# Optimization experiments

Measured on AMD Instinct MI355X. Metric: run time of the kernel, lower is better.

Reference implementation:

```python
import jax, jax.numpy as jnp
import numpy as np

N = 100000   # active voxels
C = 64       # inplanes
K3 = 27      # kernel^dim = 3^3 rulebook offsets
EPS = 1e-4   # scn.BatchNormReLU default eps


def setup_inputs() -> dict:
    key = jax.random.key(0)
    ks = jax.random.split(key, 14)
    features = jax.random.normal(ks[0], (N, C), dtype=jnp.float32)
    raw = jax.random.randint(ks[1], (N, K3), 0, 2 * N)
    neighbor_idx = jnp.where(raw < N, raw, -1).astype(jnp.int32)
    # center offset of a submanifold conv is always the site itself
    neighbor_idx = neighbor_idx.at[:, K3 // 2].set(jnp.arange(N, dtype=jnp.int32))

    def bn_params(k1, k2, k3, k4):
        gamma = 1.0 + 0.1 * jax.random.normal(k1, (C,), dtype=jnp.float32)
        beta = 0.1 * jax.random.normal(k2, (C,), dtype=jnp.float32)
        mean = 0.05 * jax.random.normal(k3, (C,), dtype=jnp.float32)
        var = 1.0 + 0.1 * jax.random.uniform(k4, (C,), dtype=jnp.float32)
        return gamma, beta, mean, var

    g1, b1, m1, v1 = bn_params(ks[2], ks[3], ks[4], ks[5])
    g2, b2, m2, v2 = bn_params(ks[6], ks[7], ks[8], ks[9])
    scale = 1.0 / np.sqrt(K3 * C)
    W1 = scale * jax.random.normal(ks[10], (K3, C, C), dtype=jnp.float32)
    W2 = scale * jax.random.normal(ks[11], (K3, C, C), dtype=jnp.float32)
    return {
        "features": features, "neighbor_idx": neighbor_idx,
        "gamma1": g1, "beta1": b1, "mean1": m1, "var1": v1, "W1": W1,
        "gamma2": g2, "beta2": b2, "mean2": m2, "var2": v2, "W2": W2,
    }


def _bn_relu(x, gamma, beta, mean, var):
    # eval-mode BatchNorm fused with ReLU, per channel
    return jax.nn.relu((x - mean) * jax.lax.rsqrt(var + EPS) * gamma + beta)


def _subm_conv(x, neighbor_idx, W):
    # gather neighbor features per rulebook offset, masked sum of per-offset GEMMs
    valid = neighbor_idx >= 0                       # [N, K3]
    g = x[jnp.where(valid, neighbor_idx, 0)]        # [N, K3, C]
    g = jnp.where(valid[..., None], g, 0.0)
    return jnp.einsum('nkc,kcd->nd', g, W)          # [N, C]


def reference(features, neighbor_idx, gamma1, beta1, mean1, var1, W1,
              gamma2, beta2, mean2, var2, W2):
    y = _bn_relu(features, gamma1, beta1, mean1, var1)
    y = _subm_conv(y, neighbor_idx, W1)
    y = _bn_relu(y, gamma2, beta2, mean2, var2)
    y = _subm_conv(y, neighbor_idx, W2)
    return features + y
```

## Files before the change

### kernel.cpp

```cpp
#include <hip/hip_runtime.h>
#include <hip/hip_bf16.h>

#define NS 100000
#define CC 64
#define K3 27
#define EPSV 1e-4f

typedef __attribute__((ext_vector_type(4))) float f32x4;
typedef __attribute__((ext_vector_type(8))) short bf16x8;

__device__ __forceinline__ short f2bf(float f) {
    union { float f; unsigned u; } uf; uf.f = f;
    unsigned r = (uf.u + 0x7fffu + ((uf.u >> 16) & 1u)) >> 16;
    return (short)r;
}

__global__ void prep_coeffs(const float* __restrict__ g1, const float* __restrict__ b1,
                            const float* __restrict__ m1, const float* __restrict__ v1,
                            const float* __restrict__ g2, const float* __restrict__ b2,
                            const float* __restrict__ m2, const float* __restrict__ v2,
                            float* __restrict__ coeffs) {
    int t = threadIdx.x;
    int ch = t & 63;
    if (t < 64) {
        float s = g1[ch] * rsqrtf(v1[ch] + EPSV);
        coeffs[ch] = s;
        coeffs[64 + ch] = b1[ch] - m1[ch] * s;
    } else {
        float s = g2[ch] * rsqrtf(v2[ch] + EPSV);
        coeffs[128 + ch] = s;
        coeffs[192 + ch] = b2[ch] - m2[ch] * s;
    }
}

__global__ void pack_w(const float* __restrict__ W1, const float* __restrict__ W2,
                       short* __restrict__ Wp1, short* __restrict__ Wp2) {
    int t = blockIdx.x * blockDim.x + threadIdx.x;
    if (t >= 2 * K3 * 8 * 64) return;
    int lane = t & 63;
    int f = t >> 6;
    int which = f / (K3 * 8);
    int f2 = f % (K3 * 8);
    int k = f2 >> 3, kc = (f2 >> 2) & 1, t4 = f2 & 3;
    const float* W = which ? W2 : W1;
    short* Wp = which ? Wp2 : Wp1;
    int col = t4 * 16 + (lane & 15);
    int kr0 = kc * 32 + 8 * (lane >> 4);
    bf16x8 v;
#pragma unroll
    for (int j = 0; j < 8; ++j) v[j] = f2bf(W[(k * CC + kr0 + j) * CC + col]);
    *(bf16x8*)(Wp + ((long)f2 * 64 + lane) * 8) = v;
}

__global__ void bn1_to_bf16(const float* __restrict__ x, const float* __restrict__ coeffs,
                            short* __restrict__ X1, short* __restrict__ X2) {
    int tid = blockIdx.x * blockDim.x + threadIdx.x;
    if (tid < NS * 8) {
        int ch8 = (tid & 7) * 8;
        const float* px = x + (long)tid * 8;
        float4 u = *(const float4*)px;
        float4 w = *(const float4*)(px + 4);
        float o[8] = {u.x, u.y, u.z, u.w, w.x, w.y, w.z, w.w};
        bf16x8 r;
#pragma unroll
        for (int j = 0; j < 8; ++j) {
            float s = coeffs[ch8 + j], bi = coeffs[64 + ch8 + j];
            float y = fmaxf(fmaf(o[j], s, bi), 0.f);
            r[j] = f2bf(y);
        }
        *(bf16x8*)(X1 + (long)tid * 8) = r;
    }
    if (blockIdx.x == 0 && threadIdx.x < 64) {
        X1[(long)NS * 64 + threadIdx.x] = 0;
        X2[(long)NS * 64 + threadIdx.x] = 0;
    }
}

template <int PHASE>
__global__ __launch_bounds__(256) void subm_conv(
    const short* __restrict__ Xg,
    const int* __restrict__ nb,
    const short* __restrict__ Wp,
    const float* __restrict__ coeffs,
    const float* __restrict__ feat,
    short* __restrict__ Xout,
    float* __restrict__ yout)
{
    int lane = threadIdx.x & 63;
    int wv = blockIdx.x * 4 + (threadIdx.x >> 6);
    int base = wv * 32;
    if (base >= NS) return;
    int r15 = lane & 15, hi = lane >> 4;
    int site0 = base + r15;
    int site1 = base + 16 + r15;

    f32x4 acc[2][4] = {};
    const bf16x8* wpv = (const bf16x8*)Wp;

    for (int k = 0; k < K3; ++k) {
        int i0 = nb[site0 * K3 + k];
        int i1 = nb[site1 * K3 + k];
        int q0 = (i0 < 0) ? NS : i0;
        int q1 = (i1 < 0) ? NS : i1;
        const short* p0 = Xg + (long)q0 * 64 + hi * 8;
        const short* p1 = Xg + (long)q1 * 64 + hi * 8;
        bf16x8 a00 = *(const bf16x8*)p0;
        bf16x8 a01 = *(const bf16x8*)(p0 + 32);
        bf16x8 a10 = *(const bf16x8*)p1;
        bf16x8 a11 = *(const bf16x8*)(p1 + 32);
        const bf16x8* bp = wpv + (long)k * 8 * 64 + lane;
#pragma unroll
        for (int t4 = 0; t4 < 4; ++t4) {
            bf16x8 b0 = bp[t4 * 64];
            bf16x8 b1 = bp[(4 + t4) * 64];
            acc[0][t4] = __builtin_amdgcn_mfma_f32_16x16x32_bf16(a00, b0, acc[0][t4], 0, 0, 0);
            acc[1][t4] = __builtin_amdgcn_mfma_f32_16x16x32_bf16(a10, b0, acc[1][t4], 0, 0, 0);
            acc[0][t4] = __builtin_amdgcn_mfma_f32_16x16x32_bf16(a01, b1, acc[0][t4], 0, 0, 0);
            acc[1][t4] = __builtin_amdgcn_mfma_f32_16x16x32_bf16(a11, b1, acc[1][t4], 0, 0, 0);
        }
    }

#pragma unroll
    for (int mt = 0; mt < 2; ++mt) {
#pragma unroll
        for (int t4 = 0; t4 < 4; ++t4) {
            int col = t4 * 16 + r15;
            float sc = 0.f, bi = 0.f;
            if (PHASE == 1) { sc = coeffs[128 + col]; bi = coeffs[192 + col]; }
#pragma unroll
            for (int r = 0; r < 4; ++r) {
                int row = base + mt * 16 + hi * 4 + r;
                long off = (long)row * 64 + col;
                float v = acc[mt][t4][r];
                if (PHASE == 1) {
                    float y = fmaxf(fmaf(v, sc, bi), 0.f);
                    Xout[off] = f2bf(y);
                } else {
                    yout[off] = feat[off] + v;
                }
            }
        }
    }
}

extern "C" void kernel_launch(void* const* d_in, const int* in_sizes, int n_in,
                              void* d_out, int out_size, void* d_ws, size_t ws_size,
                              hipStream_t stream) {
    const float* feat = (const float*)d_in[0];
    const int*   nb   = (const int*)d_in[1];
    const float* g1 = (const float*)d_in[2];
    const float* b1 = (const float*)d_in[3];
    const float* m1 = (const float*)d_in[4];
    const float* v1 = (const float*)d_in[5];
    const float* W1 = (const float*)d_in[6];
    const float* g2 = (const float*)d_in[7];
    const float* b2 = (const float*)d_in[8];
    const float* m2 = (const float*)d_in[9];
    const float* v2 = (const float*)d_in[10];
    const float* W2 = (const float*)d_in[11];
    float* out = (float*)d_out;

    char* ws = (char*)d_ws;
    short* X1 = (short*)ws;
    short* X2 = (short*)(ws + 12802048);
    short* Wp1 = (short*)(ws + 25604096);
    short* Wp2 = (short*)(ws + 25604096 + 221184);
    float* coeffs = (float*)(ws + 25604096 + 2 * 221184);

    prep_coeffs<<<1, 128, 0, stream>>>(g1, b1, m1, v1, g2, b2, m2, v2, coeffs);
    pack_w<<<108, 256, 0, stream>>>(W1, W2, Wp1, Wp2);
    bn1_to_bf16<<<3125, 256, 0, stream>>>(feat, coeffs, X1, X2);
    subm_conv<1><<<782, 256, 0, stream>>>(X1, nb, Wp1, coeffs, nullptr, X2, nullptr);
    subm_conv<2><<<782, 256, 0, stream>>>(X2, nb, Wp2, coeffs, feat, nullptr, out);
}
```

Measured before the change: 270.5 us.

## Split rulebook offsets across waves with LDS reduction and merge prep kernels

Each block now handles 32 sites, and its four waves each take a strided subset of the 27 offsets. Partial accumulators are reduced through shared memory before a vectorized epilogue. Neighbor indices are prefetched up front, and the prep, weight-pack and BN1 kernels are merged into one launch, with BN coefficients computed inline. This raises parallelism and grid size (3125 blocks instead of 782) to better hide gather latency. The cost is 32KB of LDS per block, a __syncthreads, and one padded wasted iteration for the waves whose offset index reaches 27 or more.

```diff
diff --git a/kernel.cpp b/kernel.cpp
--- a/kernel.cpp
+++ b/kernel.cpp
@@ -5,6 +5,8 @@
 #define CC 64
 #define K3 27
 #define EPSV 1e-4f
+#define NBLK 3125
+#define PACKB 108
 
 typedef __attribute__((ext_vector_type(4))) float f32x4;
 typedef __attribute__((ext_vector_type(8))) short bf16x8;
@@ -15,100 +17,108 @@
     return (short)r;
 }
 
-__global__ void prep_coeffs(const float* __restrict__ g1, const float* __restrict__ b1,
-                            const float* __restrict__ m1, const float* __restrict__ v1,
-                            const float* __restrict__ g2, const float* __restrict__ b2,
-                            const float* __restrict__ m2, const float* __restrict__ v2,
-                            float* __restrict__ coeffs) {
-    int t = threadIdx.x;
-    int ch = t & 63;
-    if (t < 64) {
-        float s = g1[ch] * rsqrtf(v1[ch] + EPSV);
-        coeffs[ch] = s;
-        coeffs[64 + ch] = b1[ch] - m1[ch] * s;
-    } else {
-        float s = g2[ch] * rsqrtf(v2[ch] + EPSV);
-        coeffs[128 + ch] = s;
-        coeffs[192 + ch] = b2[ch] - m2[ch] * s;
-    }
-}
-
-__global__ void pack_w(const float* __restrict__ W1, const float* __restrict__ W2,
-                       short* __restrict__ Wp1, short* __restrict__ Wp2) {
-    int t = blockIdx.x * blockDim.x + threadIdx.x;
-    if (t >= 2 * K3 * 8 * 64) return;
-    int lane = t & 63;
-    int f = t >> 6;
-    int which = f / (K3 * 8);
-    int f2 = f % (K3 * 8);
-    int k = f2 >> 3, kc = (f2 >> 2) & 1, t4 = f2 & 3;
-    const float* W = which ? W2 : W1;
-    short* Wp = which ? Wp2 : Wp1;
-    int col = t4 * 16 + (lane & 15);
-    int kr0 = kc * 32 + 8 * (lane >> 4);
-    bf16x8 v;
-#pragma unroll
-    for (int j = 0; j < 8; ++j) v[j] = f2bf(W[(k * CC + kr0 + j) * CC + col]);
-    *(bf16x8*)(Wp + ((long)f2 * 64 + lane) * 8) = v;
-}
-
-__global__ void bn1_to_bf16(const float* __restrict__ x, const float* __restrict__ coeffs,
-                            short* __restrict__ X1, short* __restrict__ X2) {
-    int tid = blockIdx.x * blockDim.x + threadIdx.x;
-    if (tid < NS * 8) {
+__global__ __launch_bounds__(256) void prepare(
+    const float* __restrict__ x,
+    const float* __restrict__ g1, const float* __restrict__ b1,
+    const float* __restrict__ m1, const float* __restrict__ v1,
+    const float* __restrict__ W1, const float* __restrict__ W2,
+    short* __restrict__ X1, short* __restrict__ X2,
+    short* __restrict__ Wp1, short* __restrict__ Wp2)
+{
+    int blk = blockIdx.x;
+    if (blk < NBLK) {
+        int tid = blk * 256 + threadIdx.x;
         int ch8 = (tid & 7) * 8;
+        float4 ga = *(const float4*)(g1 + ch8), gb = *(const float4*)(g1 + ch8 + 4);
+        float4 ba = *(const float4*)(b1 + ch8), bb = *(const float4*)(b1 + ch8 + 4);
+        float4 ma = *(const float4*)(m1 + ch8), mb = *(const float4*)(m1 + ch8 + 4);
+        float4 va = *(const float4*)(v1 + ch8), vb = *(const float4*)(v1 + ch8 + 4);
+        float g[8] = {ga.x,ga.y,ga.z,ga.w,gb.x,gb.y,gb.z,gb.w};
+        float b[8] = {ba.x,ba.y,ba.z,ba.w,bb.x,bb.y,bb.z,bb.w};
+        float m[8] = {ma.x,ma.y,ma.z,ma.w,mb.x,mb.y,mb.z,mb.w};
+        float vv[8] = {va.x,va.y,va.z,va.w,vb.x,vb.y,vb.z,vb.w};
         const float* px = x + (long)tid * 8;
         float4 u = *(const float4*)px;
         float4 w = *(const float4*)(px + 4);
-        float o[8] = {u.x, u.y, u.z, u.w, w.x, w.y, w.z, w.w};
+        float o[8] = {u.x,u.y,u.z,u.w,w.x,w.y,w.z,w.w};
         bf16x8 r;
 #pragma unroll
         for (int j = 0; j < 8; ++j) {
-            float s = coeffs[ch8 + j], bi = coeffs[64 + ch8 + j];
-            float y = fmaxf(fmaf(o[j], s, bi), 0.f);
-            r[j] = f2bf(y);
+            float s = g[j] * rsqrtf(vv[j] + EPSV);
+            float bi = b[j] - m[j] * s;
+            r[j] = f2bf(fmaxf(fmaf(o[j], s, bi), 0.f));
         }
         *(bf16x8*)(X1 + (long)tid * 8) = r;
-    }
-    if (blockIdx.x == 0 && threadIdx.x < 64) {
-        X1[(long)NS * 64 + threadIdx.x] = 0;
-        X2[(long)NS * 64 + threadIdx.x] = 0;
+        if (blk == 0 && threadIdx.x < 64) {
+            X1[(long)NS * 64 + threadIdx.x] = 0;
+            X2[(long)NS * 64 + threadIdx.x] = 0;
+        }
+    } else {
+        int t = (blk - NBLK) * 256 + threadIdx.x;
+        if (t >= 2 * K3 * 8 * 64) return;
+        int lane = t & 63;
+        int f = t >> 6;
+        int which = f / (K3 * 8);
+        int f2 = f % (K3 * 8);
+        int k = f2 >> 3, kc = (f2 >> 2) & 1, t4 = f2 & 3;
+        const float* W = which ? W2 : W1;
+        short* Wp = which ? Wp2 : Wp1;
+        int col = t4 * 16 + (lane & 15);
+        int kr0 = kc * 32 + 8 * (lane >> 4);
+        bf16x8 v;
+#pragma unroll
+        for (int j = 0; j < 8; ++j) v[j] = f2bf(W[(k * CC + kr0 + j) * CC + col]);
+        *(bf16x8*)(Wp + ((long)f2 * 64 + lane) * 8) = v;
     }
 }
 
 template <int PHASE>
-__global__ __launch_bounds__(256) void subm_conv(
+__global__ __launch_bounds__(256, 4) void subm_conv(
     const short* __restrict__ Xg,
     const int* __restrict__ nb,
     const short* __restrict__ Wp,
-    const float* __restrict__ coeffs,
+    const float* __restrict__ g2, const float* __restrict__ b2,
+    const float* __restrict__ m2, const float* __restrict__ v2,
     const float* __restrict__ feat,
-    short* __restrict__ Xout,
-    float* __restrict__ yout)
+    short* __restrict__ Xout, float* __restrict__ yout)
 {
+    __shared__ float red[4][32][64];
+    __shared__ float s2c[64], b2c[64];
     int lane = threadIdx.x & 63;
-    int wv = blockIdx.x * 4 + (threadIdx.x >> 6);
-    int base = wv * 32;
-    if (base >= NS) return;
+    int w = threadIdx.x >> 6;
+    int base = blockIdx.x * 32;
     int r15 = lane & 15, hi = lane >> 4;
-    int site0 = base + r15;
-    int site1 = base + 16 + r15;
+    int site0 = base + r15, site1 = base + 16 + r15;
+
+    if (PHASE == 1 && threadIdx.x < 64) {
+        float s = g2[threadIdx.x] * rsqrtf(v2[threadIdx.x] + EPSV);
+        s2c[threadIdx.x] = s;
+        b2c[threadIdx.x] = b2[threadIdx.x] - m2[threadIdx.x] * s;
+    }
+
+    int q0[7], q1[7];
+#pragma unroll
+    for (int j = 0; j < 7; ++j) {
+        int k = w + 4 * j;
+        int i0 = (k < K3) ? nb[site0 * K3 + k] : -1;
+        int i1 = (k < K3) ? nb[site1 * K3 + k] : -1;
+        q0[j] = (i0 < 0) ? NS : i0;
+        q1[j] = (i1 < 0) ? NS : i1;
+    }
 
     f32x4 acc[2][4] = {};
     const bf16x8* wpv = (const bf16x8*)Wp;
-
-    for (int k = 0; k < K3; ++k) {
-        int i0 = nb[site0 * K3 + k];
-        int i1 = nb[site1 * K3 + k];
-        int q0 = (i0 < 0) ? NS : i0;
-        int q1 = (i1 < 0) ? NS : i1;
-        const short* p0 = Xg + (long)q0 * 64 + hi * 8;
-        const short* p1 = Xg + (long)q1 * 64 + hi * 8;
+#pragma unroll
+    for (int j = 0; j < 7; ++j) {
+        int k = w + 4 * j;
+        int kk = (k < K3) ? k : 0;
+        const short* p0 = Xg + (long)q0[j] * 64 + hi * 8;
+        const short* p1 = Xg + (long)q1[j] * 64 + hi * 8;
         bf16x8 a00 = *(const bf16x8*)p0;
         bf16x8 a01 = *(const bf16x8*)(p0 + 32);
         bf16x8 a10 = *(const bf16x8*)p1;
         bf16x8 a11 = *(const bf16x8*)(p1 + 32);
-        const bf16x8* bp = wpv + (long)k * 8 * 64 + lane;
+        const bf16x8* bp = wpv + (long)kk * 8 * 64 + lane;
 #pragma unroll
         for (int t4 = 0; t4 < 4; ++t4) {
             bf16x8 b0 = bp[t4 * 64];
@@ -121,25 +131,36 @@
     }
 
 #pragma unroll
-    for (int mt = 0; mt < 2; ++mt) {
+    for (int mt = 0; mt < 2; ++mt)
 #pragma unroll
-        for (int t4 = 0; t4 < 4; ++t4) {
-            int col = t4 * 16 + r15;
-            float sc = 0.f, bi = 0.f;
-            if (PHASE == 1) { sc = coeffs[128 + col]; bi = coeffs[192 + col]; }
+        for (int t4 = 0; t4 < 4; ++t4)
 #pragma unroll
-            for (int r = 0; r < 4; ++r) {
-                int row = base + mt * 16 + hi * 4 + r;
-                long off = (long)row * 64 + col;
-                float v = acc[mt][t4][r];
-                if (PHASE == 1) {
-                    float y = fmaxf(fmaf(v, sc, bi), 0.f);
-                    Xout[off] = f2bf(y);
-                } else {
-                    yout[off] = feat[off] + v;
-                }
-            }
-        }
+            for (int r = 0; r < 4; ++r)
+                red[w][mt * 16 + hi * 4 + r][t4 * 16 + r15] = acc[mt][t4][r];
+    __syncthreads();
+
+    int t = threadIdx.x;
+    int lr = t >> 3, c0 = (t & 7) * 8;
+    int row = base + lr;
+    float s[8];
+#pragma unroll
+    for (int c = 0; c < 8; ++c)
+        s[c] = red[0][lr][c0 + c] + red[1][lr][c0 + c] +
+               red[2][lr][c0 + c] + red[3][lr][c0 + c];
+    if (PHASE == 1) {
+        bf16x8 o;
+#pragma unroll
+        for (int c = 0; c < 8; ++c)
+            o[c] = f2bf(fmaxf(fmaf(s[c], s2c[c0 + c], b2c[c0 + c]), 0.f));
+        *(bf16x8*)(Xout + (long)row * 64 + c0) = o;
+    } else {
+        const float* fp = feat + (long)row * 64 + c0;
+        float4 f0 = *(const float4*)fp, f1 = *(const float4*)(fp + 4);
+        float4 o0 = {s[0] + f0.x, s[1] + f0.y, s[2] + f0.z, s[3] + f0.w};
+        float4 o1 = {s[4] + f1.x, s[5] + f1.y, s[6] + f1.z, s[7] + f1.w};
+        float* op = yout + (long)row * 64 + c0;
+        *(float4*)op = o0;
+        *(float4*)(op + 4) = o1;
     }
 }
 
@@ -165,11 +186,11 @@
     short* X2 = (short*)(ws + 12802048);
     short* Wp1 = (short*)(ws + 25604096);
     short* Wp2 = (short*)(ws + 25604096 + 221184);
-    float* coeffs = (float*)(ws + 25604096 + 2 * 221184);
 
-    prep_coeffs<<<1, 128, 0, stream>>>(g1, b1, m1, v1, g2, b2, m2, v2, coeffs);
-    pack_w<<<108, 256, 0, stream>>>(W1, W2, Wp1, Wp2);
-    bn1_to_bf16<<<3125, 256, 0, stream>>>(feat, coeffs, X1, X2);
-    subm_conv<1><<<782, 256, 0, stream>>>(X1, nb, Wp1, coeffs, nullptr, X2, nullptr);
-    subm_conv<2><<<782, 256, 0, stream>>>(X2, nb, Wp2, coeffs, feat, nullptr, out);
+    prepare<<<NBLK + PACKB, 256, 0, stream>>>(feat, g1, b1, m1, v1, W1, W2,
+                                              X1, X2, Wp1, Wp2);
+    subm_conv<1><<<NBLK, 256, 0, stream>>>(X1, nb, Wp1, g2, b2, m2, v2,
+                                           nullptr, X2, nullptr);
+    subm_conv<2><<<NBLK, 256, 0, stream>>>(X2, nb, Wp2, g2, b2, m2, v2,
+                                           feat, nullptr, out);
 }
```

After: 227.0 us. -16.1%, faster.
